# Kernel tuning notes

Hardware: AMD Instinct MI355X
Metric: run time of the kernel (lower is better)

The kernel has to match this reference:

```python
import jax, jax.numpy as jnp
import numpy as np

N_NODES = 100000
N_EDGES = 500000
D_IN = 128
D_HID = 128
D_OUT = 128


def _sage_conv(x, src, dst, W_l, b_l, W_r, n_nodes):
    # mean aggregation of source-node features at destination nodes
    msg = jax.ops.segment_sum(x[src], dst, num_segments=n_nodes)          # [N, d_in]
    cnt = jax.ops.segment_sum(jnp.ones((src.shape[0], 1), x.dtype), dst,
                              num_segments=n_nodes)                        # [N, 1]
    agg = msg / jnp.maximum(cnt, 1.0)
    # PyG SAGEConv: lin_l(aggregated) + lin_r(self), bias on lin_l only
    return agg @ W_l + b_l + x @ W_r


def setup_inputs() -> dict:
    key = jax.random.key(0)
    ks = jax.random.split(key, 8)
    x = jax.random.normal(ks[0], (N_NODES, D_IN), dtype=jnp.float32)
    edge_index = jax.random.randint(ks[1], (2, N_EDGES), 0, N_NODES, dtype=jnp.int32)
    s1 = 1.0 / np.sqrt(D_IN)
    s2 = 1.0 / np.sqrt(D_HID)
    W_l1 = jax.random.uniform(ks[2], (D_IN, D_HID), jnp.float32, -s1, s1)
    W_r1 = jax.random.uniform(ks[3], (D_IN, D_HID), jnp.float32, -s1, s1)
    b_l1 = jnp.zeros((D_HID,), jnp.float32)
    W_l2 = jax.random.uniform(ks[4], (D_HID, D_OUT), jnp.float32, -s2, s2)
    W_r2 = jax.random.uniform(ks[5], (D_HID, D_OUT), jnp.float32, -s2, s2)
    b_l2 = jnp.zeros((D_OUT,), jnp.float32)
    return {"x": x, "edge_index": edge_index,
            "W_l1": W_l1, "b_l1": b_l1, "W_r1": W_r1,
            "W_l2": W_l2, "b_l2": b_l2, "W_r2": W_r2}


def reference(x, edge_index, W_l1, b_l1, W_r1, W_l2, b_l2, W_r2):
    src, dst = edge_index[0], edge_index[1]
    h = _sage_conv(x, src, dst, W_l1, b_l1, W_r1, N_NODES)
    h = jax.nn.relu(h)
    out = _sage_conv(h, src, dst, W_l2, b_l2, W_r2, N_NODES)
    return out
```

## Files before the change

kernel.cpp:

```cpp
#include <hip/hip_runtime.h>
#include <cstddef>

#define N_NODES 100000
#define N_EDGES 500000
#define D 128

typedef __attribute__((ext_vector_type(8))) short bf16x8;
typedef __attribute__((ext_vector_type(4))) float f32x4;

static __device__ __forceinline__ short f2bf(float f)
{
    unsigned u = __builtin_bit_cast(unsigned, f);
    unsigned r = (u + 0x7fffu + ((u >> 16) & 1u)) >> 16;
    return (short)r;
}
static __device__ __forceinline__ float b2f(short s)
{
    return __builtin_bit_cast(float, (unsigned)((unsigned short)s) << 16);
}


__global__ __launch_bounds__(256)
void hist_kernel(const int* __restrict__ dst, int* __restrict__ deg)
{
    int e = blockIdx.x * 256 + threadIdx.x;
    if (e < N_EDGES) atomicAdd(&deg[dst[e]], 1);
}

__global__ __launch_bounds__(512)
void scanA_kernel(const int* __restrict__ deg, int* __restrict__ bsum)
{
    __shared__ int s[512];
    int t = threadIdx.x;
    int idx = blockIdx.x * 512 + t;
    s[t] = (idx < N_NODES) ? deg[idx] : 0;
    __syncthreads();
    for (int off = 256; off > 0; off >>= 1) {
        if (t < off) s[t] += s[t + off];
        __syncthreads();
    }
    if (t == 0) bsum[blockIdx.x] = s[0];
}

__global__ __launch_bounds__(256)
void scanB_kernel(const int* __restrict__ bsum, int* __restrict__ boff)
{
    __shared__ int s[256];
    int t = threadIdx.x;
    int v = (t < 196) ? bsum[t] : 0;
    s[t] = v;
    __syncthreads();
    for (int off = 1; off < 256; off <<= 1) {
        int a = s[t];
        if (t >= off) a += s[t - off];
        __syncthreads();
        s[t] = a;
        __syncthreads();
    }
    if (t < 196) boff[t] = s[t] - v;
}

__global__ __launch_bounds__(512)
void scanC_kernel(const int* __restrict__ deg, const int* __restrict__ boff,
                  int* __restrict__ row_ptr, int* __restrict__ cursor)
{
    __shared__ int s[512];
    int t = threadIdx.x;
    int idx = blockIdx.x * 512 + t;
    int v = (idx < N_NODES) ? deg[idx] : 0;
    s[t] = v;
    __syncthreads();
    for (int off = 1; off < 512; off <<= 1) {
        int a = s[t];
        if (t >= off) a += s[t - off];
        __syncthreads();
        s[t] = a;
        __syncthreads();
    }
    int excl = boff[blockIdx.x] + s[t] - v;
    if (idx < N_NODES) { row_ptr[idx] = excl; cursor[idx] = excl; }
    else if (idx == N_NODES) { row_ptr[idx] = excl; }
}

__global__ __launch_bounds__(256)
void permute_kernel(const int* __restrict__ src, const int* __restrict__ dst,
                    int* __restrict__ cursor, int* __restrict__ perm)
{
    int e = blockIdx.x * 256 + threadIdx.x;
    if (e < N_EDGES) {
        int pos = atomicAdd(&cursor[dst[e]], 1);
        perm[pos] = src[e];
    }
}

__global__ __launch_bounds__(256)
void cast_kernel(const float* __restrict__ in, short* __restrict__ outb)
{
    int i = blockIdx.x * 256 + threadIdx.x;
    const float4* p = reinterpret_cast<const float4*>(in) + (size_t)i * 2;
    float4 lo = p[0], hi = p[1];
    bf16x8 v;
    v[0] = f2bf(lo.x); v[1] = f2bf(lo.y); v[2] = f2bf(lo.z); v[3] = f2bf(lo.w);
    v[4] = f2bf(hi.x); v[5] = f2bf(hi.y); v[6] = f2bf(hi.z); v[7] = f2bf(hi.w);
    *reinterpret_cast<bf16x8*>(outb + (size_t)i * 8) = v;
}

__global__ __launch_bounds__(256)
void pack_w_kernel(const float* __restrict__ Wl1, const float* __restrict__ Wr1,
                   const float* __restrict__ Wl2, const float* __restrict__ Wr2,
                   short* __restrict__ blob)
{
    int tid = blockIdx.x * 256 + threadIdx.x;
    if (tid >= 8192) return;
    int lane = tid & 63;
    int frag = (tid >> 6) & 63;
    int layer = tid >> 12;
    int cb = frag & 7;
    int ks = frag >> 3;
    int k0 = ks * 32 + (lane >> 4) * 8;
    int col = cb * 16 + (lane & 15);
    const float* Wl = layer ? Wl2 : Wl1;
    const float* Wr = layer ? Wr2 : Wr1;
    const float* W = (k0 < 128) ? (Wl + (size_t)k0 * D) : (Wr + (size_t)(k0 - 128) * D);
    bf16x8 v;
    #pragma unroll
    for (int j = 0; j < 8; ++j)
        v[j] = f2bf(W[(size_t)j * D + col]);
    *reinterpret_cast<bf16x8*>(blob + (size_t)tid * 8) = v;
}

__global__ __launch_bounds__(256)
void fused_layer_kernel(const short* __restrict__ gsrc,
                        const short* __restrict__ selfb,
                        const int* __restrict__ row_ptr,
                        const int* __restrict__ perm,
                        const short* __restrict__ blob,
                        const float* __restrict__ bias,
                        float* __restrict__ outf,
                        short* __restrict__ outb,
                        int mode)
{
    __shared__ short As[64 * 128];

    const int tid = threadIdx.x;
    const int row0 = blockIdx.x * 64;

    {
        const int c8 = (tid & 15) * 8;
        for (int p = 0; p < 4; ++p) {
            int r = p * 16 + (tid >> 4);
            int node = row0 + r;
            if (node < N_NODES) {
                int beg = row_ptr[node];
                int end = row_ptr[node + 1];
                float acc[8] = {};
                int e = beg;
                for (; e + 2 <= end; e += 2) {
                    int s0 = perm[e], s1 = perm[e + 1];
                    bf16x8 v0 = *reinterpret_cast<const bf16x8*>(gsrc + (size_t)s0 * D + c8);
                    bf16x8 v1 = *reinterpret_cast<const bf16x8*>(gsrc + (size_t)s1 * D + c8);
                    #pragma unroll
                    for (int j = 0; j < 8; ++j) acc[j] += b2f(v0[j]) + b2f(v1[j]);
                }
                if (e < end) {
                    int s0 = perm[e];
                    bf16x8 v0 = *reinterpret_cast<const bf16x8*>(gsrc + (size_t)s0 * D + c8);
                    #pragma unroll
                    for (int j = 0; j < 8; ++j) acc[j] += b2f(v0[j]);
                }
                float inv = 1.0f / fmaxf((float)(end - beg), 1.0f);
                bf16x8 o;
                #pragma unroll
                for (int j = 0; j < 8; ++j) o[j] = f2bf(acc[j] * inv);
                int idx = (r * 128 + c8) ^ ((r & 7) << 3);
                *reinterpret_cast<bf16x8*>(As + idx) = o;
            }
        }
    }
    __syncthreads();

    const int w = tid >> 6;
    const int lane = tid & 63;
    const int kch = lane >> 4;
    const int rloc = w * 16 + (lane & 15);
    int row = row0 + rloc;
    int rowc = row < N_NODES ? row : N_NODES - 1;

    const short* selfp = selfb + (size_t)rowc * D + kch * 8;

    f32x4 acc[8] = {};

    #pragma unroll
    for (int ks = 0; ks < 8; ++ks) {
        bf16x8 a;
        if (ks < 4) {
            int idx = (rloc * 128 + ks * 32 + kch * 8) ^ ((rloc & 7) << 3);
            a = *reinterpret_cast<const bf16x8*>(As + idx);
        } else {
            a = *reinterpret_cast<const bf16x8*>(selfp + (ks - 4) * 32);
        }
        const short* bptr = blob + ((size_t)(ks * 8) * 64 + lane) * 8;
        #pragma unroll
        for (int cb = 0; cb < 8; ++cb) {
            bf16x8 b = *reinterpret_cast<const bf16x8*>(bptr + (size_t)cb * 64 * 8);
            acc[cb] = __builtin_amdgcn_mfma_f32_16x16x32_bf16(a, b, acc[cb], 0, 0, 0);
        }
    }

    const int colg = lane & 15;
    const int rbase = row0 + w * 16 + (lane >> 4) * 4;
    #pragma unroll
    for (int cb = 0; cb < 8; ++cb) {
        int col = cb * 16 + colg;
        float bv = bias[col];
        #pragma unroll
        for (int r = 0; r < 4; ++r) {
            int rr = rbase + r;
            if (rr < N_NODES) {
                float v = acc[cb][r] + bv;
                if (mode) {
                    v = fmaxf(v, 0.0f);
                    outb[(size_t)rr * D + col] = f2bf(v);
                } else {
                    outf[(size_t)rr * D + col] = v;
                }
            }
        }
    }
}

extern "C" void kernel_launch(void* const* d_in, const int* in_sizes, int n_in,
                              void* d_out, int out_size, void* d_ws, size_t ws_size,
                              hipStream_t stream)
{
    const float* x   = (const float*)d_in[0];
    const int*   ei  = (const int*)d_in[1];
    const int*   src = ei;
    const int*   dst = ei + N_EDGES;
    const float* Wl1 = (const float*)d_in[2];
    const float* bl1 = (const float*)d_in[3];
    const float* Wr1 = (const float*)d_in[4];
    const float* Wl2 = (const float*)d_in[5];
    const float* bl2 = (const float*)d_in[6];
    const float* Wr2 = (const float*)d_in[7];
    float* out = (float*)d_out;

    int* deg     = (int*)d_ws;
    int* row_ptr = deg + N_NODES;
    int* cursor  = row_ptr + N_NODES + 1;
    int* bsum    = cursor + N_NODES;
    int* boff    = bsum + 256;
    int* perm    = boff + 256;
    size_t int_end = (size_t)(3 * N_NODES + 1 + 512) + N_EDGES;
    int_end = (int_end + 3) & ~(size_t)3;
    short* blob1 = (short*)((int*)d_ws + int_end);
    short* blob2 = blob1 + 32768;
    short* xb    = blob2 + 32768;
    short* hb    = xb + (size_t)N_NODES * D;

    const int edge_blocks = (N_EDGES + 255) / 256;
    const int scan_blocks = (N_NODES + 512) / 512;
    const int cast_blocks = (N_NODES * D / 8) / 256;
    const int fuse_blocks = (N_NODES + 63) / 64;

    hipMemsetAsync(deg, 0, N_NODES * sizeof(int), stream);
    hist_kernel<<<edge_blocks, 256, 0, stream>>>(dst, deg);
    scanA_kernel<<<scan_blocks, 512, 0, stream>>>(deg, bsum);
    scanB_kernel<<<1, 256, 0, stream>>>(bsum, boff);
    scanC_kernel<<<scan_blocks, 512, 0, stream>>>(deg, boff, row_ptr, cursor);
    permute_kernel<<<edge_blocks, 256, 0, stream>>>(src, dst, cursor, perm);
    cast_kernel<<<cast_blocks, 256, 0, stream>>>(x, xb);
    pack_w_kernel<<<32, 256, 0, stream>>>(Wl1, Wr1, Wl2, Wr2, blob1);

    fused_layer_kernel<<<fuse_blocks, 256, 0, stream>>>(xb, xb, row_ptr, perm,
                                                        blob1, bl1, nullptr, hb, 1);

    fused_layer_kernel<<<fuse_blocks, 256, 0, stream>>>(hb, hb, row_ptr, perm,
                                                        blob2, bl2, out, nullptr, 0);
}
```

Before: 293.4 us.

## Merge prep kernels and widen fused layer to 1024 threads per block

```diff
diff --git a/kernel.cpp b/kernel.cpp
--- a/kernel.cpp
+++ b/kernel.cpp
@@ -21,10 +21,43 @@
 
 
 __global__ __launch_bounds__(256)
-void hist_kernel(const int* __restrict__ dst, int* __restrict__ deg)
-{
-    int e = blockIdx.x * 256 + threadIdx.x;
-    if (e < N_EDGES) atomicAdd(&deg[dst[e]], 1);
+void prep_kernel(const float* __restrict__ x, short* __restrict__ xb,
+                 const int* __restrict__ dst, int* __restrict__ deg,
+                 const float* __restrict__ Wl1, const float* __restrict__ Wr1,
+                 const float* __restrict__ Wl2, const float* __restrict__ Wr2,
+                 short* __restrict__ blob)
+{
+    int gid = blockIdx.x * 256 + threadIdx.x;
+
+    {
+        const float4* p = reinterpret_cast<const float4*>(x) + (size_t)gid * 2;
+        float4 lo = p[0], hi = p[1];
+        bf16x8 v;
+        v[0] = f2bf(lo.x); v[1] = f2bf(lo.y); v[2] = f2bf(lo.z); v[3] = f2bf(lo.w);
+        v[4] = f2bf(hi.x); v[5] = f2bf(hi.y); v[6] = f2bf(hi.z); v[7] = f2bf(hi.w);
+        *reinterpret_cast<bf16x8*>(xb + (size_t)gid * 8) = v;
+    }
+
+    if (gid < N_EDGES) atomicAdd(&deg[dst[gid]], 1);
+
+    if (gid < 8192) {
+        int lane = gid & 63;
+        int frag = (gid >> 6) & 63;
+        int layer = gid >> 12;
+        int cb = frag & 7;
+        int ks = frag >> 3;
+        int k0 = ks * 32 + (lane >> 4) * 8;
+        int col = cb * 16 + (lane & 15);
+        const float* Wl = layer ? Wl2 : Wl1;
+        const float* Wr = layer ? Wr2 : Wr1;
+        const float* W = (k0 < 128) ? (Wl + (size_t)k0 * D)
+                                    : (Wr + (size_t)(k0 - 128) * D);
+        bf16x8 v;
+        #pragma unroll
+        for (int j = 0; j < 8; ++j)
+            v[j] = f2bf(W[(size_t)j * D + col]);
+        *reinterpret_cast<bf16x8*>(blob + (size_t)gid * 8) = v;
+    }
 }
 
 __global__ __launch_bounds__(512)
@@ -93,43 +126,7 @@
     }
 }
 
-__global__ __launch_bounds__(256)
-void cast_kernel(const float* __restrict__ in, short* __restrict__ outb)
-{
-    int i = blockIdx.x * 256 + threadIdx.x;
-    const float4* p = reinterpret_cast<const float4*>(in) + (size_t)i * 2;
-    float4 lo = p[0], hi = p[1];
-    bf16x8 v;
-    v[0] = f2bf(lo.x); v[1] = f2bf(lo.y); v[2] = f2bf(lo.z); v[3] = f2bf(lo.w);
-    v[4] = f2bf(hi.x); v[5] = f2bf(hi.y); v[6] = f2bf(hi.z); v[7] = f2bf(hi.w);
-    *reinterpret_cast<bf16x8*>(outb + (size_t)i * 8) = v;
-}
-
-__global__ __launch_bounds__(256)
-void pack_w_kernel(const float* __restrict__ Wl1, const float* __restrict__ Wr1,
-                   const float* __restrict__ Wl2, const float* __restrict__ Wr2,
-                   short* __restrict__ blob)
-{
-    int tid = blockIdx.x * 256 + threadIdx.x;
-    if (tid >= 8192) return;
-    int lane = tid & 63;
-    int frag = (tid >> 6) & 63;
-    int layer = tid >> 12;
-    int cb = frag & 7;
-    int ks = frag >> 3;
-    int k0 = ks * 32 + (lane >> 4) * 8;
-    int col = cb * 16 + (lane & 15);
-    const float* Wl = layer ? Wl2 : Wl1;
-    const float* Wr = layer ? Wr2 : Wr1;
-    const float* W = (k0 < 128) ? (Wl + (size_t)k0 * D) : (Wr + (size_t)(k0 - 128) * D);
-    bf16x8 v;
-    #pragma unroll
-    for (int j = 0; j < 8; ++j)
-        v[j] = f2bf(W[(size_t)j * D + col]);
-    *reinterpret_cast<bf16x8*>(blob + (size_t)tid * 8) = v;
-}
-
-__global__ __launch_bounds__(256)
+__global__ __launch_bounds__(1024)
 void fused_layer_kernel(const short* __restrict__ gsrc,
                         const short* __restrict__ selfb,
                         const int* __restrict__ row_ptr,
@@ -146,35 +143,33 @@
     const int row0 = blockIdx.x * 64;
 
     {
+        const int r = tid >> 4;
         const int c8 = (tid & 15) * 8;
-        for (int p = 0; p < 4; ++p) {
-            int r = p * 16 + (tid >> 4);
-            int node = row0 + r;
-            if (node < N_NODES) {
-                int beg = row_ptr[node];
-                int end = row_ptr[node + 1];
-                float acc[8] = {};
-                int e = beg;
-                for (; e + 2 <= end; e += 2) {
-                    int s0 = perm[e], s1 = perm[e + 1];
-                    bf16x8 v0 = *reinterpret_cast<const bf16x8*>(gsrc + (size_t)s0 * D + c8);
-                    bf16x8 v1 = *reinterpret_cast<const bf16x8*>(gsrc + (size_t)s1 * D + c8);
-                    #pragma unroll
-                    for (int j = 0; j < 8; ++j) acc[j] += b2f(v0[j]) + b2f(v1[j]);
-                }
-                if (e < end) {
-                    int s0 = perm[e];
-                    bf16x8 v0 = *reinterpret_cast<const bf16x8*>(gsrc + (size_t)s0 * D + c8);
-                    #pragma unroll
-                    for (int j = 0; j < 8; ++j) acc[j] += b2f(v0[j]);
-                }
-                float inv = 1.0f / fmaxf((float)(end - beg), 1.0f);
-                bf16x8 o;
+        int node = row0 + r;
+        if (node < N_NODES) {
+            int beg = row_ptr[node];
+            int end = row_ptr[node + 1];
+            float acc[8] = {};
+            int e = beg;
+            for (; e + 2 <= end; e += 2) {
+                int s0 = perm[e], s1 = perm[e + 1];
+                bf16x8 v0 = *reinterpret_cast<const bf16x8*>(gsrc + (size_t)s0 * D + c8);
+                bf16x8 v1 = *reinterpret_cast<const bf16x8*>(gsrc + (size_t)s1 * D + c8);
                 #pragma unroll
-                for (int j = 0; j < 8; ++j) o[j] = f2bf(acc[j] * inv);
-                int idx = (r * 128 + c8) ^ ((r & 7) << 3);
-                *reinterpret_cast<bf16x8*>(As + idx) = o;
+                for (int j = 0; j < 8; ++j) acc[j] += b2f(v0[j]) + b2f(v1[j]);
             }
+            if (e < end) {
+                int s0 = perm[e];
+                bf16x8 v0 = *reinterpret_cast<const bf16x8*>(gsrc + (size_t)s0 * D + c8);
+                #pragma unroll
+                for (int j = 0; j < 8; ++j) acc[j] += b2f(v0[j]);
+            }
+            float inv = 1.0f / fmaxf((float)(end - beg), 1.0f);
+            bf16x8 o;
+            #pragma unroll
+            for (int j = 0; j < 8; ++j) o[j] = f2bf(acc[j] * inv);
+            int idx = (r * 128 + c8) ^ ((r & 7) << 3);
+            *reinterpret_cast<bf16x8*>(As + idx) = o;
         }
     }
     __syncthreads();
@@ -182,13 +177,15 @@
     const int w = tid >> 6;
     const int lane = tid & 63;
     const int kch = lane >> 4;
-    const int rloc = w * 16 + (lane & 15);
+    const int rg = w & 3;
+    const int cb0 = (w >> 2) * 2;
+    const int rloc = rg * 16 + (lane & 15);
     int row = row0 + rloc;
     int rowc = row < N_NODES ? row : N_NODES - 1;
 
     const short* selfp = selfb + (size_t)rowc * D + kch * 8;
 
-    f32x4 acc[8] = {};
+    f32x4 acc[2] = {};
 
     #pragma unroll
     for (int ks = 0; ks < 8; ++ks) {
@@ -199,25 +196,24 @@
         } else {
             a = *reinterpret_cast<const bf16x8*>(selfp + (ks - 4) * 32);
         }
-        const short* bptr = blob + ((size_t)(ks * 8) * 64 + lane) * 8;
-        #pragma unroll
-        for (int cb = 0; cb < 8; ++cb) {
-            bf16x8 b = *reinterpret_cast<const bf16x8*>(bptr + (size_t)cb * 64 * 8);
-            acc[cb] = __builtin_amdgcn_mfma_f32_16x16x32_bf16(a, b, acc[cb], 0, 0, 0);
-        }
+        const short* bptr = blob + ((size_t)(ks * 8 + cb0) * 64 + lane) * 8;
+        bf16x8 b0 = *reinterpret_cast<const bf16x8*>(bptr);
+        bf16x8 b1 = *reinterpret_cast<const bf16x8*>(bptr + 64 * 8);
+        acc[0] = __builtin_amdgcn_mfma_f32_16x16x32_bf16(a, b0, acc[0], 0, 0, 0);
+        acc[1] = __builtin_amdgcn_mfma_f32_16x16x32_bf16(a, b1, acc[1], 0, 0, 0);
     }
 
     const int colg = lane & 15;
-    const int rbase = row0 + w * 16 + (lane >> 4) * 4;
+    const int rbase = row0 + rg * 16 + (lane >> 4) * 4;
     #pragma unroll
-    for (int cb = 0; cb < 8; ++cb) {
-        int col = cb * 16 + colg;
+    for (int i = 0; i < 2; ++i) {
+        int col = (cb0 + i) * 16 + colg;
         float bv = bias[col];
         #pragma unroll
         for (int r = 0; r < 4; ++r) {
             int rr = rbase + r;
             if (rr < N_NODES) {
-                float v = acc[cb][r] + bv;
+                float v = acc[i][r] + bv;
                 if (mode) {
                     v = fmaxf(v, 0.0f);
                     outb[(size_t)rr * D + col] = f2bf(v);
@@ -260,21 +256,20 @@
 
     const int edge_blocks = (N_EDGES + 255) / 256;
     const int scan_blocks = (N_NODES + 512) / 512;
-    const int cast_blocks = (N_NODES * D / 8) / 256;
+    const int prep_blocks = (N_NODES * D / 8) / 256;
     const int fuse_blocks = (N_NODES + 63) / 64;
 
     hipMemsetAsync(deg, 0, N_NODES * sizeof(int), stream);
-    hist_kernel<<<edge_blocks, 256, 0, stream>>>(dst, deg);
+    prep_kernel<<<prep_blocks, 256, 0, stream>>>(x, xb, dst, deg,
+                                                 Wl1, Wr1, Wl2, Wr2, blob1);
     scanA_kernel<<<scan_blocks, 512, 0, stream>>>(deg, bsum);
     scanB_kernel<<<1, 256, 0, stream>>>(bsum, boff);
     scanC_kernel<<<scan_blocks, 512, 0, stream>>>(deg, boff, row_ptr, cursor);
     permute_kernel<<<edge_blocks, 256, 0, stream>>>(src, dst, cursor, perm);
-    cast_kernel<<<cast_blocks, 256, 0, stream>>>(x, xb);
-    pack_w_kernel<<<32, 256, 0, stream>>>(Wl1, Wr1, Wl2, Wr2, blob1);
-
-    fused_layer_kernel<<<fuse_blocks, 256, 0, stream>>>(xb, xb, row_ptr, perm,
-                                                        blob1, bl1, nullptr, hb, 1);
-
-    fused_layer_kernel<<<fuse_blocks, 256, 0, stream>>>(hb, hb, row_ptr, perm,
-                                                        blob2, bl2, out, nullptr, 0);
-}
+
+    fused_layer_kernel<<<fuse_blocks, 1024, 0, stream>>>(xb, xb, row_ptr, perm,
+                                                         blob1, bl1, nullptr, hb, 1);
+
+    fused_layer_kernel<<<fuse_blocks, 1024, 0, stream>>>(hb, hb, row_ptr, perm,
+                                                         blob2, bl2, out, nullptr, 0);
+}
```

New measurement: 288.0 us. No clear change (-1.8%).
